# Performance work log

Measured on AMD Instinct MI355X. Metric: run time of the kernel, lower is better.

## Reference

```python
import jax, jax.numpy as jnp
import numpy as np

B = 64        # number of queries (eg_idx)
E = 1024      # edges per query (contiguous blocks)
N = B * E     # total edges
M = 65536     # number of visited nodes
D = 128       # n_dims_in
D4 = 4 * D    # G3 concat dim


def setup_inputs():
    key = jax.random.key(0)
    ks = jax.random.split(key, 12)
    std = np.sqrt(2.0 / D4).astype(np.float32)
    visited_node_score = jax.random.uniform(ks[0], (M,), dtype=jnp.float32)
    visited_node_representation = jax.random.normal(ks[1], (M, D), dtype=jnp.float32)
    rel_emb = jax.random.normal(ks[2], (N, D), dtype=jnp.float32)
    query_src_ts_emb = jax.random.normal(ks[3], (B, D), dtype=jnp.float32)
    query_rel_emb = jax.random.normal(ks[4], (B, D), dtype=jnp.float32)
    Wq = jax.random.normal(ks[5], (D4, D4), dtype=jnp.float32) * std
    Wk = jax.random.normal(ks[6], (D4, D4), dtype=jnp.float32) * std
    # edges: (eg_idx, vi, ti, vj, tj, rel, node_idx_i, node_idx_j)
    eg_idx = jnp.repeat(jnp.arange(B, dtype=jnp.int32), E)          # sorted by query
    node_i = jnp.sort(jax.random.randint(ks[7], (N,), 0, M, dtype=jnp.int32))  # contiguous segments
    node_j = jax.random.randint(ks[8], (N,), 0, M, dtype=jnp.int32)
    dummy = jax.random.randint(ks[9], (N, 4), 0, M, dtype=jnp.int32)
    edges = jnp.concatenate([eg_idx[:, None], dummy[:, :3], dummy[:, 3:4],
                             jnp.zeros((N, 1), jnp.int32), node_i[:, None], node_j[:, None]], axis=1)
    return {
        'visited_node_score': visited_node_score,
        'visited_node_representation': visited_node_representation,
        'rel_emb': rel_emb,
        'query_src_ts_emb': query_src_ts_emb,
        'query_rel_emb': query_rel_emb,
        'Wq': Wq,
        'Wk': Wk,
        'edges': edges,
        'max_edges': 64,
    }


def _attention_flow(visited_node_score, visited_node_representation, rel_emb,
                    query_src_ts_emb, query_rel_emb, Wq, Wk, edges, max_edges):
    seg = edges[:, 6]            # node_idx_i: segment ids (contiguous blocks)
    eg = edges[:, 0]             # query index
    hvi = visited_node_representation[seg]           # [N, D]
    hvj = visited_node_representation[edges[:, 7]]   # [N, D]
    qs = query_src_ts_emb[eg]                        # [N, D]
    qr = query_rel_emb[eg]                           # [N, D]
    left = jnp.concatenate([hvi, rel_emb, qs, qr], axis=-1)   # [N, 4D]
    right = jnp.concatenate([hvj, rel_emb, qs, qr], axis=-1)  # [N, 4D]
    # G3 bilinear score: sum(query_proj(left) * key_proj(right), -1)
    logits = jnp.sum((left @ Wq.T) * (right @ Wk.T), axis=-1)  # [N]
    # segment softmax over node_idx_i segments
    smax = jax.ops.segment_max(logits, seg, num_segments=M)
    ex = jnp.exp(logits - smax[seg])
    den = jax.ops.segment_sum(ex, seg, num_segments=M)
    soft = ex / den[seg]                                       # [N]
    src_score = visited_node_score[seg]
    target_score = soft * src_score                            # [N]
    # per-query top-k pruning (edges are contiguous per query)
    vals, idx = jax.lax.top_k(target_score.reshape(B, E), max_edges)  # [B, k]
    orig_indices = (idx + jnp.arange(B, dtype=idx.dtype)[:, None] * E).reshape(-1)
    pruned_target_score = vals.reshape(-1)
    pruned_softmax = soft[orig_indices]
    pruned_edges = edges[orig_indices]
    return pruned_target_score, pruned_softmax, pruned_edges, orig_indices


def reference(visited_node_score, visited_node_representation, rel_emb,
              query_src_ts_emb, query_rel_emb, Wq, Wk, edges, max_edges):
    return _attention_flow(visited_node_score, visited_node_representation, rel_emb,
                           query_src_ts_emb, query_rel_emb, Wq, Wk, edges, max_edges)
```

## Files before the change

### kernel.cpp

```cpp
#include <hip/hip_runtime.h>
#include <math.h>

#define NN 65536
#define KTOP 64

typedef const __attribute__((address_space(1))) void* gas_ptr;
typedef __attribute__((address_space(3))) void* las_ptr;

__device__ __forceinline__ void gload_lds16(const float* g, float* lds) {
    __builtin_amdgcn_global_load_lds((gas_ptr)g, (las_ptr)lds, 16, 0, 0);
}

__global__ void k_gemm_G(const float* __restrict__ Wq, const float* __restrict__ Wk,
                         float* __restrict__ G, float* __restrict__ Gimg)
{
    __shared__ float As[32][33];
    __shared__ float Bs[32][33];
    const int t  = threadIdx.x;
    const int tm = t >> 4, tn = t & 15;
    const int m0 = (blockIdx.x >> 4) * 32, n0 = (blockIdx.x & 15) * 32;
    float a00 = 0.f, a01 = 0.f, a10 = 0.f, a11 = 0.f;
    for (int d0 = 0; d0 < 512; d0 += 32) {
        for (int i = t; i < 1024; i += 256) {
            int r = i >> 5, c = i & 31;
            As[r][c] = Wq[(size_t)(d0 + r) * 512 + m0 + c];
            Bs[r][c] = Wk[(size_t)(d0 + r) * 512 + n0 + c];
        }
        __syncthreads();
        #pragma unroll 8
        for (int k = 0; k < 32; ++k) {
            float x0 = As[k][tm * 2], x1 = As[k][tm * 2 + 1];
            float y0 = Bs[k][tn * 2], y1 = Bs[k][tn * 2 + 1];
            a00 += x0 * y0; a01 += x0 * y1; a10 += x1 * y0; a11 += x1 * y1;
        }
        __syncthreads();
    }
    const int mA = m0 + tm * 2, nA = n0 + tn * 2;
    G[(size_t)(mA + 0) * 512 + nA + 0] = a00;
    G[(size_t)(mA + 0) * 512 + nA + 1] = a01;
    G[(size_t)(mA + 1) * 512 + nA + 0] = a10;
    G[(size_t)(mA + 1) * 512 + nA + 1] = a11;
    if (m0 < 256 && n0 < 256) {
        auto img = [&](int m, int n, float v) {
            int kk = m & 127, c = n & 63;
            int tile = ((m >> 7) << 2) | (n >> 6);
            int x = c ^ (((kk & 7) << 3) ^ (((kk >> 6) & 1) << 2));
            Gimg[tile * 8192 + kk * 64 + x] = v;
        };
        img(mA, nA, a00); img(mA, nA + 1, a01);
        img(mA + 1, nA, a10); img(mA + 1, nA + 1, a11);
    }
}

__global__ void k_batch(const float* __restrict__ qs, const float* __restrict__ qr,
                        const float* __restrict__ G,
                        float* __restrict__ bL, float* __restrict__ bR, float* __restrict__ cB)
{
    const int e = blockIdx.x, t = threadIdx.x;
    __shared__ float qcat[256];
    __shared__ float whi[256];
    __shared__ float red[256];
    qcat[t] = (t < 128) ? qs[(size_t)e * 128 + t] : qr[(size_t)e * 128 + (t - 128)];
    __syncthreads();
    float w0 = 0.f, w1 = 0.f;
    for (int r = 0; r < 256; ++r) {
        float q = qcat[r];
        w0 += G[(size_t)t * 512 + 256 + r] * q;
        w1 += G[(size_t)(t + 256) * 512 + 256 + r] * q;
    }
    bL[(size_t)e * 256 + t] = w0;
    whi[t] = w1;
    float v = 0.f;
    for (int r = 0; r < 256; ++r)
        v += qcat[r] * G[(size_t)(256 + r) * 512 + t];
    bR[(size_t)e * 256 + t] = v;
    __syncthreads();
    red[t] = qcat[t] * whi[t];
    __syncthreads();
    for (int s = 128; s > 0; s >>= 1) {
        if (t < s) red[t] += red[t + s];
        __syncthreads();
    }
    if (t == 0) cB[e] = red[0];
}

#define FMAROW(J, AX) \
    acc[J][0] += AX * b0.x; acc[J][1] += AX * b0.y; \
    acc[J][2] += AX * b0.z; acc[J][3] += AX * b0.w; \
    acc[J][4] += AX * b1.x; acc[J][5] += AX * b1.y; \
    acc[J][6] += AX * b1.z; acc[J][7] += AX * b1.w;

__launch_bounds__(256, 2)
__global__ void k_edge(const float* __restrict__ vnr, const float* __restrict__ rel,
                       const int* __restrict__ edges, const float* __restrict__ Gimg,
                       const float* __restrict__ bL, const float* __restrict__ bR,
                       const float* __restrict__ cB, float* __restrict__ logits)
{
    __shared__ __align__(16) float At[128][64];
    __shared__ __align__(16) float Bt[128][64];
    __shared__ __align__(16) float bLs[256];
    __shared__ __align__(16) float bRs[256];
    __shared__ int jL[64];

    const int t  = threadIdx.x;
    const int n0 = blockIdx.x * 64;
    const int eg = n0 >> 10;

    const int kh = t & 1;
    const int g  = (t >> 1) & 7;
    const int p  = t >> 4;
    const int e0 = 4 * p;
    const int eS = t & 63, w = t >> 6;
    float* BtF = &Bt[0][0];

    if (t < 64) jL[t] = edges[(size_t)(n0 + t) * 8 + 7];
    bLs[t] = bL[(size_t)eg * 256 + t];
    bRs[t] = bR[(size_t)eg * 256 + t];

    {
        int seg = edges[(size_t)(n0 + eS) * 8 + 6];
        const float* src = vnr + (size_t)seg * 128 + w * 32;
        float4 a[8];
        #pragma unroll
        for (int q = 0; q < 8; ++q) a[q] = *(const float4*)(src + q * 4);
        #pragma unroll
        for (int q = 0; q < 8; ++q) {
            int k = w * 32 + q * 4;
            At[k + 0][eS] = a[q].x; At[k + 1][eS] = a[q].y;
            At[k + 2][eS] = a[q].z; At[k + 3][eS] = a[q].w;
        }
    }
    __syncthreads();

    double s[4] = {0.0, 0.0, 0.0, 0.0};

    for (int kt = 0; kt < 2; ++kt) {
        if (kt == 1) {
            const float* src = rel + (size_t)(n0 + eS) * 128 + w * 32;
            float4 a[8];
            #pragma unroll
            for (int q = 0; q < 8; ++q) a[q] = *(const float4*)(src + q * 4);
            __syncthreads();
            #pragma unroll
            for (int q = 0; q < 8; ++q) {
                int k = w * 32 + q * 4;
                At[k + 0][eS] = a[q].x; At[k + 1][eS] = a[q].y;
                At[k + 2][eS] = a[q].z; At[k + 3][eS] = a[q].w;
            }
            __syncthreads();
        }
        {
            const int kb = (t & 15) * 8;
            float la[4] = {0.f, 0.f, 0.f, 0.f};
            #pragma unroll
            for (int i = 0; i < 8; ++i) {
                float bl = bLs[kt * 128 + kb + i];
                float4 a = *(const float4*)&At[kb + i][e0];
                la[0] += a.x * bl; la[1] += a.y * bl;
                la[2] += a.z * bl; la[3] += a.w * bl;
            }
            #pragma unroll
            for (int j = 0; j < 4; ++j) s[j] += (double)la[j];
        }

        for (int ct = 0; ct < 4; ++ct) {
            if (ct > 0) __syncthreads();
            {
                const int tile = kt * 4 + ct;
                const float* gsrc = Gimg + tile * 8192 + w * 256 + (t & 63) * 4;
                float* ldst = BtF + w * 256;
                #pragma unroll
                for (int r = 0; r < 8; ++r)
                    gload_lds16(gsrc + r * 1024, ldst + r * 1024);
            }
            float4 rpre[8];
            #pragma unroll
            for (int j = 0; j < 4; ++j) {
                const float* rp = (ct < 2)
                    ? (vnr + (size_t)jL[e0 + j] * 128 + ct * 64 + g * 8)
                    : (rel + (size_t)(n0 + e0 + j) * 128 + (ct - 2) * 64 + g * 8);
                rpre[2 * j]     = *(const float4*)(rp);
                rpre[2 * j + 1] = *(const float4*)(rp + 4);
            }
            __syncthreads();
            float acc[4][8] = {};
            const int cb0 = (g * 8) ^ (kh << 2);
            #pragma unroll 8
            for (int i = 0; i < 64; ++i) {
                const int kk = kh * 64 + i;
                float4 a  = *(const float4*)&At[kk][e0];
                const int cb = cb0 ^ ((i & 7) << 3);
                float4 b0 = *(const float4*)&Bt[kk][cb];
                float4 b1 = *(const float4*)&Bt[kk][cb ^ 4];
                FMAROW(0, a.x) FMAROW(1, a.y) FMAROW(2, a.z) FMAROW(3, a.w)
            }
            const int cbase = ct * 64 + g * 8;
            const bool doBR = (kt == 0) && (kh == 0);
            float4 br0, br1;
            if (doBR) {
                br0 = *(const float4*)&bRs[cbase];
                br1 = *(const float4*)&bRs[cbase + 4];
            }
            #pragma unroll
            for (int j = 0; j < 4; ++j) {
                float4 ra = rpre[2 * j], rb = rpre[2 * j + 1];
                float d = acc[j][0] * ra.x + acc[j][1] * ra.y + acc[j][2] * ra.z + acc[j][3] * ra.w
                        + acc[j][4] * rb.x + acc[j][5] * rb.y + acc[j][6] * rb.z + acc[j][7] * rb.w;
                if (doBR) {
                    d += ra.x * br0.x + ra.y * br0.y + ra.z * br0.z + ra.w * br0.w
                       + rb.x * br1.x + rb.y * br1.y + rb.z * br1.z + rb.w * br1.w;
                }
                s[j] += (double)d;
            }
        }
    }
    #pragma unroll
    for (int m = 1; m < 16; m <<= 1) {
        #pragma unroll
        for (int j = 0; j < 4; ++j) s[j] += __shfl_xor(s[j], m, 64);
    }
    if ((t & 15) == 0) {
        float base = cB[eg];
        #pragma unroll
        for (int j = 0; j < 4; ++j)
            logits[n0 + e0 + j] = (float)s[j] + base;
    }
}

__global__ void k_segstats(const int* __restrict__ edges, const float* __restrict__ logits,
                           const float* __restrict__ score,
                           float* __restrict__ soft, float* __restrict__ tsc)
{
    int n = blockIdx.x * 256 + threadIdx.x;
    if (n >= NN) return;
    int s = edges[(size_t)n * 8 + 6];
    if (n > 0 && edges[(size_t)(n - 1) * 8 + 6] == s) return;
    float m = -INFINITY;
    int k = n;
    while (k < NN && edges[(size_t)k * 8 + 6] == s) {
        m = fmaxf(m, logits[k]);
        ++k;
    }
    float d = 0.f;
    for (int q = n; q < k; ++q) d += expf(logits[q] - m);
    float sc = score[s];
    for (int q = n; q < k; ++q) {
        float so = expf(logits[q] - m) / d;
        soft[q] = so;
        tsc[q]  = so * sc;
    }
}

__global__ void k_topk(const int* __restrict__ edges, const float* __restrict__ soft,
                       const float* __restrict__ tsc, float* __restrict__ out)
{
    __shared__ float vsh[1024];
    __shared__ int   ish[1024];
    const int r = blockIdx.x, t = threadIdx.x;
    const int n = r * 1024 + t;
    float v = tsc[n];
    int idx = t;
    for (int size = 2; size <= 1024; size <<= 1) {
        for (int stride = size >> 1; stride > 0; stride >>= 1) {
            float v2; int i2;
            if (stride < 64) {
                v2 = __shfl_xor(v, stride, 64);
                i2 = __shfl_xor(idx, stride, 64);
            } else {
                __syncthreads();
                vsh[t] = v; ish[t] = idx;
                __syncthreads();
                v2 = vsh[t ^ stride]; i2 = ish[t ^ stride];
            }
            bool before = (v > v2) || (v == v2 && idx < i2);
            bool desc   = ((t & size) == 0);
            bool keep   = ((t & stride) == 0) ? (before == desc) : (before != desc);
            if (!keep) { v = v2; idx = i2; }
        }
    }
    if (t < KTOP) {
        int orig = r * 1024 + idx;
        int o = r * KTOP + t;
        out[o]        = v;
        out[4096 + o] = soft[orig];
        #pragma unroll
        for (int q = 0; q < 8; ++q)
            out[8192 + (size_t)o * 8 + q] = (float)edges[(size_t)orig * 8 + q];
        out[40960 + o] = (float)orig;
    }
}

extern "C" void kernel_launch(void* const* d_in, const int* in_sizes, int n_in,
                              void* d_out, int out_size, void* d_ws, size_t ws_size,
                              hipStream_t stream)
{
    (void)in_sizes; (void)n_in; (void)out_size; (void)ws_size;
    const float* score = (const float*)d_in[0];
    const float* vnr   = (const float*)d_in[1];
    const float* rel   = (const float*)d_in[2];
    const float* qs    = (const float*)d_in[3];
    const float* qr    = (const float*)d_in[4];
    const float* Wq    = (const float*)d_in[5];
    const float* Wk    = (const float*)d_in[6];
    const int*   edges = (const int*)  d_in[7];
    float* out = (float*)d_out;

    float* ws     = (float*)d_ws;
    float* G      = ws;
    float* Gimg   = G      + 262144;
    float* bL     = Gimg   + 65536;
    float* bR     = bL     + 16384;
    float* cB     = bR     + 16384;
    float* logits = cB     + 64;
    float* soft   = logits + 65536;
    float* tsc    = soft   + 65536;

    k_gemm_G  <<<256, 256, 0, stream>>>(Wq, Wk, G, Gimg);
    k_batch   <<<64, 256, 0, stream>>>(qs, qr, G, bL, bR, cB);
    k_edge    <<<1024, 256, 0, stream>>>(vnr, rel, edges, Gimg, bL, bR, cB, logits);
    k_segstats<<<256, 256, 0, stream>>>(edges, logits, score, soft, tsc);
    k_topk    <<<64, 1024, 0, stream>>>(edges, soft, tsc, out);
}
```

Measured before the change: 308.1 us.

## Double-buffer G tiles in edge kernel, swizzle LDS, and retile G GEMM

The edge kernel now streams G in 64x64 half-tiles through a double-buffered LDS region, prefetching the next tile with async global-to-LDS loads while computing on the current one. It also XOR-swizzles the At layout to cut bank conflicts and lowers the launch bounds to one block per CU. The G GEMM moves to 64x64 tiles with 4x4 register blocking, float4 loads and register prefetch, and the Gimg image is re-laid-out to match. The k_batch reduction uses float4 loads. Lower occupancy and the 16-phase loop with one barrier per phase may cost latency hiding.

```diff
diff --git a/kernel.cpp b/kernel.cpp
--- a/kernel.cpp
+++ b/kernel.cpp
@@ -14,41 +14,61 @@
 __global__ void k_gemm_G(const float* __restrict__ Wq, const float* __restrict__ Wk,
                          float* __restrict__ G, float* __restrict__ Gimg)
 {
-    __shared__ float As[32][33];
-    __shared__ float Bs[32][33];
+    __shared__ __align__(16) float As[32][68];
+    __shared__ __align__(16) float Bs[32][68];
     const int t  = threadIdx.x;
     const int tm = t >> 4, tn = t & 15;
-    const int m0 = (blockIdx.x >> 4) * 32, n0 = (blockIdx.x & 15) * 32;
-    float a00 = 0.f, a01 = 0.f, a10 = 0.f, a11 = 0.f;
-    for (int d0 = 0; d0 < 512; d0 += 32) {
-        for (int i = t; i < 1024; i += 256) {
-            int r = i >> 5, c = i & 31;
-            As[r][c] = Wq[(size_t)(d0 + r) * 512 + m0 + c];
-            Bs[r][c] = Wk[(size_t)(d0 + r) * 512 + n0 + c];
-        }
+    const int m0 = (blockIdx.x >> 3) * 64, n0 = (blockIdx.x & 7) * 64;
+    const int sr = t >> 3, sc = (t & 7) * 8;
+
+    float4 q0, q1, v0, v1;
+    {
+        const float* wq = Wq + (size_t)sr * 512 + m0 + sc;
+        const float* wk = Wk + (size_t)sr * 512 + n0 + sc;
+        q0 = *(const float4*)wq; q1 = *(const float4*)(wq + 4);
+        v0 = *(const float4*)wk; v1 = *(const float4*)(wk + 4);
+    }
+    float acc[4][4] = {};
+    for (int k0 = 0; k0 < 512; k0 += 32) {
         __syncthreads();
+        *(float4*)&As[sr][sc]     = q0; *(float4*)&As[sr][sc + 4] = q1;
+        *(float4*)&Bs[sr][sc]     = v0; *(float4*)&Bs[sr][sc + 4] = v1;
+        __syncthreads();
+        if (k0 + 32 < 512) {
+            const float* wq = Wq + (size_t)(k0 + 32 + sr) * 512 + m0 + sc;
+            const float* wk = Wk + (size_t)(k0 + 32 + sr) * 512 + n0 + sc;
+            q0 = *(const float4*)wq; q1 = *(const float4*)(wq + 4);
+            v0 = *(const float4*)wk; v1 = *(const float4*)(wk + 4);
+        }
         #pragma unroll 8
         for (int k = 0; k < 32; ++k) {
-            float x0 = As[k][tm * 2], x1 = As[k][tm * 2 + 1];
-            float y0 = Bs[k][tn * 2], y1 = Bs[k][tn * 2 + 1];
-            a00 += x0 * y0; a01 += x0 * y1; a10 += x1 * y0; a11 += x1 * y1;
-        }
-        __syncthreads();
-    }
-    const int mA = m0 + tm * 2, nA = n0 + tn * 2;
-    G[(size_t)(mA + 0) * 512 + nA + 0] = a00;
-    G[(size_t)(mA + 0) * 512 + nA + 1] = a01;
-    G[(size_t)(mA + 1) * 512 + nA + 0] = a10;
-    G[(size_t)(mA + 1) * 512 + nA + 1] = a11;
+            float4 a = *(const float4*)&As[k][tm * 4];
+            float4 b = *(const float4*)&Bs[k][tn * 4];
+            acc[0][0] += a.x*b.x; acc[0][1] += a.x*b.y; acc[0][2] += a.x*b.z; acc[0][3] += a.x*b.w;
+            acc[1][0] += a.y*b.x; acc[1][1] += a.y*b.y; acc[1][2] += a.y*b.z; acc[1][3] += a.y*b.w;
+            acc[2][0] += a.z*b.x; acc[2][1] += a.z*b.y; acc[2][2] += a.z*b.z; acc[2][3] += a.z*b.w;
+            acc[3][0] += a.w*b.x; acc[3][1] += a.w*b.y; acc[3][2] += a.w*b.z; acc[3][3] += a.w*b.w;
+        }
+    }
+    #pragma unroll
+    for (int im = 0; im < 4; ++im) {
+        int m = m0 + tm * 4 + im;
+        float4 o; o.x = acc[im][0]; o.y = acc[im][1]; o.z = acc[im][2]; o.w = acc[im][3];
+        *(float4*)&G[(size_t)m * 512 + n0 + tn * 4] = o;
+    }
     if (m0 < 256 && n0 < 256) {
-        auto img = [&](int m, int n, float v) {
-            int kk = m & 127, c = n & 63;
-            int tile = ((m >> 7) << 2) | (n >> 6);
-            int x = c ^ (((kk & 7) << 3) ^ (((kk >> 6) & 1) << 2));
-            Gimg[tile * 8192 + kk * 64 + x] = v;
-        };
-        img(mA, nA, a00); img(mA, nA + 1, a01);
-        img(mA + 1, nA, a10); img(mA + 1, nA + 1, a11);
+        #pragma unroll
+        for (int im = 0; im < 4; ++im) {
+            int m = m0 + tm * 4 + im;
+            int r = m & 63;
+            #pragma unroll
+            for (int in = 0; in < 4; ++in) {
+                int n = n0 + tn * 4 + in;
+                int T = ((m >> 6) << 2) | (n >> 6);
+                int x = (n & 63) ^ ((r & 7) << 3) ^ (((r >> 5) & 1) << 2);
+                Gimg[T * 4096 + r * 64 + x] = acc[im][in];
+            }
+        }
     }
 }
 
@@ -57,16 +77,18 @@
                         float* __restrict__ bL, float* __restrict__ bR, float* __restrict__ cB)
 {
     const int e = blockIdx.x, t = threadIdx.x;
-    __shared__ float qcat[256];
+    __shared__ __align__(16) float qcat[256];
     __shared__ float whi[256];
     __shared__ float red[256];
     qcat[t] = (t < 128) ? qs[(size_t)e * 128 + t] : qr[(size_t)e * 128 + (t - 128)];
     __syncthreads();
     float w0 = 0.f, w1 = 0.f;
-    for (int r = 0; r < 256; ++r) {
-        float q = qcat[r];
-        w0 += G[(size_t)t * 512 + 256 + r] * q;
-        w1 += G[(size_t)(t + 256) * 512 + 256 + r] * q;
+    for (int r4 = 0; r4 < 64; ++r4) {
+        float4 g0 = *(const float4*)&G[(size_t)t * 512 + 256 + r4 * 4];
+        float4 g1 = *(const float4*)&G[(size_t)(t + 256) * 512 + 256 + r4 * 4];
+        float4 q  = *(const float4*)&qcat[r4 * 4];
+        w0 += g0.x*q.x + g0.y*q.y + g0.z*q.z + g0.w*q.w;
+        w1 += g1.x*q.x + g1.y*q.y + g1.z*q.z + g1.w*q.w;
     }
     bL[(size_t)e * 256 + t] = w0;
     whi[t] = w1;
@@ -90,14 +112,14 @@
     acc[J][4] += AX * b1.x; acc[J][5] += AX * b1.y; \
     acc[J][6] += AX * b1.z; acc[J][7] += AX * b1.w;
 
-__launch_bounds__(256, 2)
+__launch_bounds__(256, 1)
 __global__ void k_edge(const float* __restrict__ vnr, const float* __restrict__ rel,
                        const int* __restrict__ edges, const float* __restrict__ Gimg,
                        const float* __restrict__ bL, const float* __restrict__ bR,
                        const float* __restrict__ cB, float* __restrict__ logits)
 {
     __shared__ __align__(16) float At[128][64];
-    __shared__ __align__(16) float Bt[128][64];
+    __shared__ __align__(16) float Bt[2][64][64];
     __shared__ __align__(16) float bLs[256];
     __shared__ __align__(16) float bRs[256];
     __shared__ int jL[64];
@@ -108,15 +130,21 @@
 
     const int kh = t & 1;
     const int g  = (t >> 1) & 7;
-    const int p  = t >> 4;
-    const int e0 = 4 * p;
+    const int e0 = 4 * (t >> 4);
     const int eS = t & 63, w = t >> 6;
-    float* BtF = &Bt[0][0];
+    const int ldsOfs = w * 256;
 
     if (t < 64) jL[t] = edges[(size_t)(n0 + t) * 8 + 7];
     bLs[t] = bL[(size_t)eg * 256 + t];
     bRs[t] = bR[(size_t)eg * 256 + t];
 
+    {
+        const float* gsrc = Gimg + t * 4;
+        float* ldst = &Bt[0][0][0] + ldsOfs;
+        #pragma unroll
+        for (int q = 0; q < 4; ++q)
+            gload_lds16(gsrc + q * 1024, ldst + q * 1024);
+    }
     {
         int seg = edges[(size_t)(n0 + eS) * 8 + 6];
         const float* src = vnr + (size_t)seg * 128 + w * 32;
@@ -126,93 +154,116 @@
         #pragma unroll
         for (int q = 0; q < 8; ++q) {
             int k = w * 32 + q * 4;
-            At[k + 0][eS] = a[q].x; At[k + 1][eS] = a[q].y;
-            At[k + 2][eS] = a[q].z; At[k + 3][eS] = a[q].w;
+            int col = eS ^ (((k >> 3) & 15) << 2);
+            At[k + 0][col] = a[q].x; At[k + 1][col] = a[q].y;
+            At[k + 2][col] = a[q].z; At[k + 3][col] = a[q].w;
         }
     }
     __syncthreads();
 
     double s[4] = {0.0, 0.0, 0.0, 0.0};
 
-    for (int kt = 0; kt < 2; ++kt) {
-        if (kt == 1) {
+    {
+        const int kb = (t & 15) * 8;
+        const int colA = e0 ^ ((t & 15) << 2);
+        float la[4] = {0.f, 0.f, 0.f, 0.f};
+        #pragma unroll
+        for (int i = 0; i < 8; ++i) {
+            float bl = bLs[kb + i];
+            float4 a = *(const float4*)&At[kb + i][colA];
+            la[0] += a.x * bl; la[1] += a.y * bl;
+            la[2] += a.z * bl; la[3] += a.w * bl;
+        }
+        #pragma unroll
+        for (int j = 0; j < 4; ++j) s[j] += (double)la[j];
+    }
+
+    int cur = 0;
+    float4 arel[8];
+
+    #pragma unroll 1
+    for (int ph = 0; ph < 16; ++ph) {
+        const int kt2 = ph >> 2, ct = ph & 3;
+        if (ph < 15) {
+            const float* gsrc = Gimg + (ph + 1) * 4096 + t * 4;
+            float* ldst = &Bt[cur ^ 1][0][0] + ldsOfs;
+            #pragma unroll
+            for (int q = 0; q < 4; ++q)
+                gload_lds16(gsrc + q * 1024, ldst + q * 1024);
+        }
+        float4 rpre[8];
+        #pragma unroll
+        for (int j = 0; j < 4; ++j) {
+            const float* rp = (ct < 2)
+                ? (vnr + (size_t)jL[e0 + j] * 128 + ct * 64 + g * 8)
+                : (rel + (size_t)(n0 + e0 + j) * 128 + (ct - 2) * 64 + g * 8);
+            rpre[2 * j]     = *(const float4*)(rp);
+            rpre[2 * j + 1] = *(const float4*)(rp + 4);
+        }
+        if (ph == 7) {
             const float* src = rel + (size_t)(n0 + eS) * 128 + w * 32;
-            float4 a[8];
-            #pragma unroll
-            for (int q = 0; q < 8; ++q) a[q] = *(const float4*)(src + q * 4);
-            __syncthreads();
+            #pragma unroll
+            for (int q = 0; q < 8; ++q) arel[q] = *(const float4*)(src + q * 4);
+        }
+        float acc[4][8] = {};
+        const int cb0   = (g * 8) ^ (kh << 2);
+        const int rbase = (kt2 & 1) * 64 + kh * 32;
+        const float* btb = &Bt[cur][0][0] + kh * 32 * 64;
+        #pragma unroll
+        for (int m = 0; m < 4; ++m) {
+            const int colA = e0 ^ ((((rbase >> 3) + m) & 15) << 2);
+            #pragma unroll
+            for (int jj = 0; jj < 8; ++jj) {
+                const int i = m * 8 + jj;
+                float4 a  = *(const float4*)&At[rbase + i][colA];
+                const int cb = cb0 ^ (jj << 3);
+                float4 b0 = *(const float4*)(btb + i * 64 + cb);
+                float4 b1 = *(const float4*)(btb + i * 64 + (cb ^ 4));
+                FMAROW(0, a.x) FMAROW(1, a.y) FMAROW(2, a.z) FMAROW(3, a.w)
+            }
+        }
+        const int cbase = ct * 64 + g * 8;
+        const bool doBR = (kt2 == 0) && (kh == 0);
+        float4 br0, br1;
+        if (doBR) {
+            br0 = *(const float4*)&bRs[cbase];
+            br1 = *(const float4*)&bRs[cbase + 4];
+        }
+        #pragma unroll
+        for (int j = 0; j < 4; ++j) {
+            float4 ra = rpre[2 * j], rb = rpre[2 * j + 1];
+            float d = acc[j][0]*ra.x + acc[j][1]*ra.y + acc[j][2]*ra.z + acc[j][3]*ra.w
+                    + acc[j][4]*rb.x + acc[j][5]*rb.y + acc[j][6]*rb.z + acc[j][7]*rb.w;
+            if (doBR) {
+                d += ra.x*br0.x + ra.y*br0.y + ra.z*br0.z + ra.w*br0.w
+                   + rb.x*br1.x + rb.y*br1.y + rb.z*br1.z + rb.w*br1.w;
+            }
+            s[j] += (double)d;
+        }
+        __syncthreads();
+        if (ph == 7) {
             #pragma unroll
             for (int q = 0; q < 8; ++q) {
                 int k = w * 32 + q * 4;
-                At[k + 0][eS] = a[q].x; At[k + 1][eS] = a[q].y;
-                At[k + 2][eS] = a[q].z; At[k + 3][eS] = a[q].w;
+                int col = eS ^ (((k >> 3) & 15) << 2);
+                At[k + 0][col] = arel[q].x; At[k + 1][col] = arel[q].y;
+                At[k + 2][col] = arel[q].z; At[k + 3][col] = arel[q].w;
             }
             __syncthreads();
-        }
-        {
             const int kb = (t & 15) * 8;
+            const int colA = e0 ^ ((t & 15) << 2);
             float la[4] = {0.f, 0.f, 0.f, 0.f};
             #pragma unroll
             for (int i = 0; i < 8; ++i) {
-                float bl = bLs[kt * 128 + kb + i];
-                float4 a = *(const float4*)&At[kb + i][e0];
+                float bl = bLs[128 + kb + i];
+                float4 a = *(const float4*)&At[kb + i][colA];
                 la[0] += a.x * bl; la[1] += a.y * bl;
                 la[2] += a.z * bl; la[3] += a.w * bl;
             }
             #pragma unroll
             for (int j = 0; j < 4; ++j) s[j] += (double)la[j];
         }
-
-        for (int ct = 0; ct < 4; ++ct) {
-            if (ct > 0) __syncthreads();
-            {
-                const int tile = kt * 4 + ct;
-                const float* gsrc = Gimg + tile * 8192 + w * 256 + (t & 63) * 4;
-                float* ldst = BtF + w * 256;
-                #pragma unroll
-                for (int r = 0; r < 8; ++r)
-                    gload_lds16(gsrc + r * 1024, ldst + r * 1024);
-            }
-            float4 rpre[8];
-            #pragma unroll
-            for (int j = 0; j < 4; ++j) {
-                const float* rp = (ct < 2)
-                    ? (vnr + (size_t)jL[e0 + j] * 128 + ct * 64 + g * 8)
-                    : (rel + (size_t)(n0 + e0 + j) * 128 + (ct - 2) * 64 + g * 8);
-                rpre[2 * j]     = *(const float4*)(rp);
-                rpre[2 * j + 1] = *(const float4*)(rp + 4);
-            }
-            __syncthreads();
-            float acc[4][8] = {};
-            const int cb0 = (g * 8) ^ (kh << 2);
-            #pragma unroll 8
-            for (int i = 0; i < 64; ++i) {
-                const int kk = kh * 64 + i;
-                float4 a  = *(const float4*)&At[kk][e0];
-                const int cb = cb0 ^ ((i & 7) << 3);
-                float4 b0 = *(const float4*)&Bt[kk][cb];
-                float4 b1 = *(const float4*)&Bt[kk][cb ^ 4];
-                FMAROW(0, a.x) FMAROW(1, a.y) FMAROW(2, a.z) FMAROW(3, a.w)
-            }
-            const int cbase = ct * 64 + g * 8;
-            const bool doBR = (kt == 0) && (kh == 0);
-            float4 br0, br1;
-            if (doBR) {
-                br0 = *(const float4*)&bRs[cbase];
-                br1 = *(const float4*)&bRs[cbase + 4];
-            }
-            #pragma unroll
-            for (int j = 0; j < 4; ++j) {
-                float4 ra = rpre[2 * j], rb = rpre[2 * j + 1];
-                float d = acc[j][0] * ra.x + acc[j][1] * ra.y + acc[j][2] * ra.z + acc[j][3] * ra.w
-                        + acc[j][4] * rb.x + acc[j][5] * rb.y + acc[j][6] * rb.z + acc[j][7] * rb.w;
-                if (doBR) {
-                    d += ra.x * br0.x + ra.y * br0.y + ra.z * br0.z + ra.w * br0.w
-                       + rb.x * br1.x + rb.y * br1.y + rb.z * br1.z + rb.w * br1.w;
-                }
-                s[j] += (double)d;
-            }
-        }
+        cur ^= 1;
     }
     #pragma unroll
     for (int m = 1; m < 16; m <<= 1) {
@@ -315,7 +366,7 @@
     float* soft   = logits + 65536;
     float* tsc    = soft   + 65536;
 
-    k_gemm_G  <<<256, 256, 0, stream>>>(Wq, Wk, G, Gimg);
+    k_gemm_G  <<<64, 256, 0, stream>>>(Wq, Wk, G, Gimg);
     k_batch   <<<64, 256, 0, stream>>>(qs, qr, G, bL, bR, cB);
     k_edge    <<<1024, 256, 0, stream>>>(vnr, rel, edges, Gimg, bL, bR, cB, logits);
     k_segstats<<<256, 256, 0, stream>>>(edges, logits, score, soft, tsc);
```

Measured after the change: 709.9 us. 2.3x slower.
